# Kernel optimization log

Measured on AMD Instinct MI355X. Metric: run time of the kernel, lower is better.

The kernel has to match this reference:

```python
import jax, jax.numpy as jnp
import numpy as np

B, T, CH_IN = 4096, 8, 2048
C, N, K = 1024, 512, 5  # chennel, prototype length, n_prototypes/classes
EPS = 1e-8


def setup_inputs() -> dict:
    key = jax.random.key(0)
    ks = jax.random.split(key, 14)
    rn = lambda k, s: jax.random.normal(k, s, dtype=jnp.float32)
    return {
        "x": rn(ks[0], (B, T, CH_IN)),
        "static": rn(ks[1], (K, CH_IN, N)),
        "Wk": rn(ks[2], (C, CH_IN)) * 0.02, "bk": rn(ks[3], (C,)) * 0.02,
        "Wv": rn(ks[4], (C, CH_IN)) * 0.02, "bv": rn(ks[5], (C,)) * 0.02,
        "WEk": rn(ks[6], (C, CH_IN)) * 0.02, "bEk": rn(ks[7], (C,)) * 0.02,
        "WEv": rn(ks[8], (C, CH_IN)) * 0.02, "bEv": rn(ks[9], (C,)) * 0.02,
        "Ww": rn(ks[10], (1, C)) * 0.02, "bw": rn(ks[11], (1,)) * 0.02,
        "Wout": rn(ks[12], (K, 2 * C)) * 0.02, "bout": rn(ks[13], (K,)) * 0.02,
    }


def reference(x, static, Wk, bk, Wv, bv, WEk, bEk, WEv, bEv, Ww, bw, Wout, bout):
    # last frame only: [B, ch_in]
    x_last = x[:, -1, :]
    # 1x1 convs on a length-1 sequence == plain linear layers
    k = x_last @ Wk.T + bk  # [B, C]
    v = x_last @ Wv.T + bv  # [B, C]
    # project all 5 static prototypes at once: [K, C, N]
    Ek = jnp.einsum('ci,kin->kcn', WEk, static) + bEk[None, :, None]
    Ev = jnp.einsum('ci,kin->kcn', WEv, static) + bEv[None, :, None]
    # cosine similarity along channel dim (torch eps=1e-8)
    kn = k / jnp.maximum(jnp.linalg.norm(k, axis=1, keepdims=True), EPS)
    Ekn = Ek / jnp.maximum(jnp.linalg.norm(Ek, axis=1, keepdims=True), EPS)
    sim = jnp.einsum('bc,kcn->bkn', kn, Ekn)          # [B, K, N]
    w = jax.nn.softmax(sim, axis=-1)                  # softmax over prototypes' N entries
    # weighted sum of Ev per prototype -> feature_E [B, C, K]
    feature_E = jnp.einsum('kcn,bkn->bck', Ev, w)
    # scalar gate per prototype via conv2_1_W, then sigmoid
    fw = jax.nn.sigmoid(jnp.einsum('c,bck->bk', Ww[0], feature_E) + bw[0])  # [B, K]
    fE = jnp.einsum('bck,bk->bc', feature_E, fw)      # [B, C]
    out = jax.nn.relu(jnp.concatenate([v, fE], axis=1))  # [B, 2C]
    out = out @ Wout.T + bout                          # [B, K]
    return out[:, :, None]                             # [B, K, 1] matching torch conv1d output
```

## Files before the change

### kernel.cpp

```cpp
#include <hip/hip_runtime.h>
#include <hip/hip_bf16.h>

#define BB 4096
#define TT 8
#define CHIN 2048
#define CC 1024
#define NN 512
#define KK 5
#define KN (KK*NN)

typedef __bf16 bf16x8 __attribute__((ext_vector_type(8)));
typedef float  f32x4  __attribute__((ext_vector_type(4)));

#define BM 256
#define BN 256

__device__ __forceinline__ void gload_lds16(const __hip_bfloat16* g, __hip_bfloat16* l) {
    __builtin_amdgcn_global_load_lds(
        (__attribute__((address_space(1))) void*)const_cast<__hip_bfloat16*>(g),
        (__attribute__((address_space(3))) void*)l, 16, 0, 0);
}

__device__ __forceinline__ void stage_q(const __hip_bfloat16* __restrict__ g, int ldg,
                                        __hip_bfloat16* l, int tid)
{
    const int P   = tid * 16;
    const int row = P >> 7;
    const int bc  = (P & 127) ^ ((row & 7) << 4);
    gload_lds16(g + (size_t)row * ldg + (bc >> 1),
                (__hip_bfloat16*)((char*)l + P));
}

__device__ __forceinline__ int xcd_remap()
{
    const int gx = gridDim.x, gy = gridDim.y, gz = gridDim.z;
    const int lin = blockIdx.x + gx * (blockIdx.y + gy * blockIdx.z);
    const int nwg = gx * gy * gz;
    return (lin & 7) * (nwg >> 3) + (lin >> 3);
}

__device__ __forceinline__ void gemm8p_body(
    const __hip_bfloat16* __restrict__ Ag, int lda,
    const __hip_bfloat16* __restrict__ Bg, int ldb,
    float* __restrict__ Cmat, int ldc,
    int ntiles,
    const float* __restrict__ bias_col,
    int bm, int bn)
{
    __shared__ __align__(16) __hip_bfloat16 As[2][BM * 64];
    __shared__ __align__(16) __hip_bfloat16 Bs[2][BN * 64];

    const int tid  = threadIdx.x;
    const int wave = tid >> 6;
    const int lane = tid & 63;
    const int wrow = (wave >> 2) * 128;
    const int wcol = (wave & 3) * 64;
    const int fr   = lane & 15;
    const int kb0  = (lane >> 4) * 16;

    const __hip_bfloat16* Arow = Ag + (size_t)bm * lda;
    const __hip_bfloat16* Brow = Bg + (size_t)bn * ldb;

    const int rA = wrow + fr, rB = wcol + fr;
    const int swA = (rA & 7) << 4, swB = (rB & 7) << 4;
    const int offA0 = rA * 128 + ((kb0     ) ^ swA);
    const int offA1 = rA * 128 + ((kb0 + 64) ^ swA);
    const int offB0 = rB * 128 + ((kb0     ) ^ swB);
    const int offB1 = rB * 128 + ((kb0 + 64) ^ swB);

    f32x4 acc[8][4];
    #pragma unroll
    for (int i = 0; i < 8; ++i)
        #pragma unroll
        for (int j = 0; j < 4; ++j)
            acc[i][j] = {0.f, 0.f, 0.f, 0.f};

    bf16x8 a[4][2];
    bf16x8 b01[2][2];
    bf16x8 b23[2][2];

    #pragma unroll
    for (int q = 0; q < 4; ++q)
        stage_q(Arow + (size_t)(64 * q) * lda, lda, &As[0][q * 4096], tid);
    #pragma unroll
    for (int q = 0; q < 4; ++q)
        stage_q(Brow + (size_t)(64 * q) * ldb, ldb, &Bs[0][q * 4096], tid);
    if (ntiles > 1) {
        #pragma unroll
        for (int q = 0; q < 4; ++q)
            stage_q(Arow + (size_t)(64 * q) * lda + 64, lda, &As[1][q * 4096], tid);
        #pragma unroll
        for (int q = 0; q < 4; ++q)
            stage_q(Brow + (size_t)(64 * q) * ldb + 64, ldb, &Bs[1][q * 4096], tid);
        asm volatile("s_waitcnt vmcnt(8)" ::: "memory");
    } else {
        asm volatile("s_waitcnt vmcnt(0)" ::: "memory");
    }
    __builtin_amdgcn_s_barrier();
    __builtin_amdgcn_sched_barrier(0);

    for (int T = 0; T < ntiles; ++T) {
        const char* aB = (const char*)&As[T & 1][0];
        const char* bB = (const char*)&Bs[T & 1][0];
        const char* aK0 = aB + offA0; const char* aK1 = aB + offA1;
        const char* bK0 = bB + offB0; const char* bK1 = bB + offB1;
        const bool pf = (T + 2 < ntiles);
        const int  kc = (T + 2) * 64;

        #pragma unroll
        for (int i = 0; i < 4; ++i) {
            a[i][0] = *(const bf16x8*)(aK0 + i * 2048);
            a[i][1] = *(const bf16x8*)(aK1 + i * 2048);
        }
        #pragma unroll
        for (int j = 0; j < 2; ++j) {
            b01[j][0] = *(const bf16x8*)(bK0 + j * 2048);
            b01[j][1] = *(const bf16x8*)(bK1 + j * 2048);
        }
        __builtin_amdgcn_s_barrier();
        asm volatile("s_waitcnt lgkmcnt(0)" ::: "memory");
        __builtin_amdgcn_sched_barrier(0);
        __builtin_amdgcn_s_setprio(1);
        #pragma unroll
        for (int i = 0; i < 4; ++i)
            #pragma unroll
            for (int j = 0; j < 2; ++j)
                #pragma unroll
                for (int k2 = 0; k2 < 2; ++k2)
                    acc[i][j] = __builtin_amdgcn_mfma_f32_16x16x32_bf16(
                        a[i][k2], b01[j][k2], acc[i][j], 0, 0, 0);
        __builtin_amdgcn_s_setprio(0);
        __builtin_amdgcn_s_barrier();
        __builtin_amdgcn_sched_barrier(0);

        #pragma unroll
        for (int j = 0; j < 2; ++j) {
            b23[j][0] = *(const bf16x8*)(bK0 + (j + 2) * 2048);
            b23[j][1] = *(const bf16x8*)(bK1 + (j + 2) * 2048);
        }
        if (pf) {
            stage_q(Arow + kc,                       lda, &As[T & 1][0],        tid);
            stage_q(Arow + (size_t)128 * lda + kc,   lda, &As[T & 1][2 * 4096], tid);
        }
        __builtin_amdgcn_s_barrier();
        asm volatile("s_waitcnt lgkmcnt(0)" ::: "memory");
        __builtin_amdgcn_sched_barrier(0);
        __builtin_amdgcn_s_setprio(1);
        #pragma unroll
        for (int i = 0; i < 4; ++i)
            #pragma unroll
            for (int j = 0; j < 2; ++j)
                #pragma unroll
                for (int k2 = 0; k2 < 2; ++k2)
                    acc[i][j + 2] = __builtin_amdgcn_mfma_f32_16x16x32_bf16(
                        a[i][k2], b23[j][k2], acc[i][j + 2], 0, 0, 0);
        __builtin_amdgcn_s_setprio(0);
        __builtin_amdgcn_s_barrier();
        __builtin_amdgcn_sched_barrier(0);

        #pragma unroll
        for (int i = 0; i < 4; ++i) {
            a[i][0] = *(const bf16x8*)(aK0 + 8192 + i * 2048);
            a[i][1] = *(const bf16x8*)(aK1 + 8192 + i * 2048);
        }
        if (pf) {
            #pragma unroll
            for (int q = 0; q < 4; ++q)
                stage_q(Brow + (size_t)(64 * q) * ldb + kc, ldb, &Bs[T & 1][q * 4096], tid);
        }
        __builtin_amdgcn_s_barrier();
        asm volatile("s_waitcnt lgkmcnt(0)" ::: "memory");
        __builtin_amdgcn_sched_barrier(0);
        __builtin_amdgcn_s_setprio(1);
        #pragma unroll
        for (int i = 0; i < 4; ++i)
            #pragma unroll
            for (int j = 0; j < 2; ++j)
                #pragma unroll
                for (int k2 = 0; k2 < 2; ++k2)
                    acc[i + 4][j + 2] = __builtin_amdgcn_mfma_f32_16x16x32_bf16(
                        a[i][k2], b23[j][k2], acc[i + 4][j + 2], 0, 0, 0);
        __builtin_amdgcn_s_setprio(0);
        __builtin_amdgcn_s_barrier();
        __builtin_amdgcn_sched_barrier(0);

        if (pf) {
            stage_q(Arow + (size_t)64 * lda + kc,    lda, &As[T & 1][4096],     tid);
            stage_q(Arow + (size_t)192 * lda + kc,   lda, &As[T & 1][3 * 4096], tid);
            asm volatile("s_waitcnt vmcnt(8)" ::: "memory");
        } else if (T + 1 < ntiles) {
            asm volatile("s_waitcnt vmcnt(0)" ::: "memory");
        }
        __builtin_amdgcn_s_barrier();
        __builtin_amdgcn_sched_barrier(0);
        __builtin_amdgcn_s_setprio(1);
        #pragma unroll
        for (int i = 0; i < 4; ++i)
            #pragma unroll
            for (int j = 0; j < 2; ++j)
                #pragma unroll
                for (int k2 = 0; k2 < 2; ++k2)
                    acc[i + 4][j] = __builtin_amdgcn_mfma_f32_16x16x32_bf16(
                        a[i][k2], b01[j][k2], acc[i + 4][j], 0, 0, 0);
        __builtin_amdgcn_s_setprio(0);
        __builtin_amdgcn_s_barrier();
        __builtin_amdgcn_sched_barrier(0);
    }

    const int quad = lane >> 4;
    #pragma unroll
    for (int i = 0; i < 8; ++i) {
        #pragma unroll
        for (int j = 0; j < 4; ++j) {
            const int col = bn + wcol + j * 16 + fr;
            const float bc = bias_col ? bias_col[col] : 0.f;
            #pragma unroll
            for (int r = 0; r < 4; ++r) {
                const int row = bm + wrow + i * 16 + quad * 4 + r;
                Cmat[(size_t)row * ldc + col] = acc[i][j][r] + bc;
            }
        }
    }
}

__global__ __launch_bounds__(512) void gemm8p_dual(
    const __hip_bfloat16* __restrict__ A0, const __hip_bfloat16* __restrict__ B0,
    float* __restrict__ C0, const float* __restrict__ bias0, int mt0,
    const __hip_bfloat16* __restrict__ A1, const __hip_bfloat16* __restrict__ B1,
    float* __restrict__ C1, const float* __restrict__ bias1)
{
    const int W  = xcd_remap();
    const int bx = W % gridDim.x;
    const int by = W / gridDim.x;
    const bool s = by >= mt0;
    gemm8p_body(s ? A1 : A0, CHIN, s ? B1 : B0, CHIN,
                s ? C1 : C0, 2 * CC, CHIN / 64,
                s ? bias1 : bias0,
                (s ? by - mt0 : by) * BM, bx * BN);
}

__global__ __launch_bounds__(512) void gemm8p(
    const __hip_bfloat16* __restrict__ A, int lda,
    const __hip_bfloat16* __restrict__ BT, int ldb,
    float* __restrict__ C, int ldc, int ntiles,
    const float* __restrict__ bias)
{
    const int W  = xcd_remap();
    const int bx = W % gridDim.x;
    const int by = W / gridDim.x;
    gemm8p_body(A, lda, BT, ldb, C, ldc, ntiles, bias, by * BM, bx * BN);
}

__global__ __launch_bounds__(512) void gemm8p_splitk4(
    const __hip_bfloat16* __restrict__ A, int lda,
    const __hip_bfloat16* __restrict__ BT, int ldb,
    float* __restrict__ C0, float* __restrict__ C1,
    float* __restrict__ C2, float* __restrict__ C3,
    int ldc, int kq_tiles)
{
    const int W   = xcd_remap();
    const int gxy = gridDim.x * gridDim.y;
    const int z   = W / gxy;
    const int rem = W % gxy;
    const int bx  = rem % gridDim.x;
    const int by  = rem / gridDim.x;
    float* C = (z == 0) ? C0 : (z == 1) ? C1 : (z == 2) ? C2 : C3;
    gemm8p_body(A + (size_t)z * kq_tiles * 64, lda,
                BT + (size_t)z * kq_tiles * 64, ldb,
                C, ldc, kq_tiles, nullptr,
                by * BM, bx * BN);
}

#define WG ((CC*CHIN)/4)
#define XG ((BB*CHIN)/4)
#define PREP_BLOCKS ((4*WG + XG + 1024) / 256)

__device__ __forceinline__ void store_bf4(__hip_bfloat16* dst, float4 vv) {
    union { __hip_bfloat16 h[4]; unsigned long long u; } pk;
    pk.h[0] = (__hip_bfloat16)vv.x; pk.h[1] = (__hip_bfloat16)vv.y;
    pk.h[2] = (__hip_bfloat16)vv.z; pk.h[3] = (__hip_bfloat16)vv.w;
    *(unsigned long long*)dst = pk.u;
}

__global__ __launch_bounds__(256) void prep_flat(
    const float* __restrict__ Wk, const float* __restrict__ Wv,
    const float* __restrict__ WEk, const float* __restrict__ WEv,
    const float* __restrict__ x,
    const float* __restrict__ bk, const float* __restrict__ bv,
    const float* __restrict__ bEk, const float* __restrict__ bEv,
    __hip_bfloat16* __restrict__ Wkvb, __hip_bfloat16* __restrict__ WEkvb,
    __hip_bfloat16* __restrict__ xb,
    float* __restrict__ bkv, float* __restrict__ bEkv)
{
    const int gidx = blockIdx.x * 256 + threadIdx.x;
    if (gidx < 4 * WG) {
        const int mat = gidx >> 19;
        const int off = (gidx & (WG - 1)) * 4;
        const float* src = (mat == 0) ? Wk : (mat == 1) ? Wv : (mat == 2) ? WEk : WEv;
        __hip_bfloat16* dst = (mat < 2) ? (Wkvb + (size_t)mat * (CC * CHIN))
                                        : (WEkvb + (size_t)(mat - 2) * (CC * CHIN));
        store_bf4(dst + off, *(const float4*)(src + off));
    } else if (gidx < 4 * WG + XG) {
        const int off = (gidx - 4 * WG) * 4;
        const int b = off >> 11;
        const int i = off & (CHIN - 1);
        store_bf4(xb + off, *(const float4*)(x + ((size_t)b * TT + TT - 1) * CHIN + i));
    } else {
        const int off = (gidx - 4 * WG - XG) * 4;
        #pragma unroll
        for (int e = 0; e < 4; ++e) {
            const int t = off + e;
            if (t < 2 * CC) bkv[t]  = (t < CC) ? bk[t] : bv[t - CC];
            else { const int u2 = t - 2 * CC; bEkv[u2] = (u2 < CC) ? bEk[u2] : bEv[u2 - CC]; }
        }
    }
}

__global__ void transpose_static(const float* __restrict__ st,
                                 __hip_bfloat16* __restrict__ stT)
{
    __shared__ float tile[32][33];
    const int k  = blockIdx.z;
    const int i0 = blockIdx.x * 32;
    const int n0 = blockIdx.y * 32;
    const int tx = threadIdx.x, ty = threadIdx.y;
    #pragma unroll
    for (int r = 0; r < 32; r += 8)
        tile[ty + r][tx] = st[((size_t)k * CHIN + i0 + ty + r) * NN + n0 + tx];
    __syncthreads();
    #pragma unroll
    for (int r = 0; r < 32; r += 8)
        stT[((size_t)k * NN + n0 + ty + r) * CHIN + i0 + tx] = (__hip_bfloat16)tile[tx][ty + r];
}

__global__ void transpose_Ev(const float* __restrict__ Ekv,
                             __hip_bfloat16* __restrict__ EvC)
{
    __shared__ float tile[32][33];
    const int c0  = blockIdx.x * 32;
    const int kn0 = blockIdx.y * 32;
    const int tx = threadIdx.x, ty = threadIdx.y;
    #pragma unroll
    for (int r = 0; r < 32; r += 8)
        tile[ty + r][tx] = Ekv[(size_t)(kn0 + ty + r) * (2 * CC) + CC + c0 + tx];
    __syncthreads();
    #pragma unroll
    for (int r = 0; r < 32; r += 8)
        EvC[(size_t)(c0 + ty + r) * KN + kn0 + tx] = (__hip_bfloat16)tile[tx][ty + r];
}

__global__ __launch_bounds__(256) void norm_prep_E(const float* __restrict__ Ekv,
                                                   const float* __restrict__ Ww,
                                                   __hip_bfloat16* __restrict__ EknT,
                                                   float* __restrict__ g)
{
    const int kn = blockIdx.x;
    const int t  = threadIdx.x;
    const float* pk = Ekv + (size_t)kn * (2 * CC);
    const float4 ek = ((const float4*)pk)[t];
    const float4 ev = ((const float4*)(pk + CC))[t];
    const float4 ww = ((const float4*)Ww)[t];
    float s2 = ek.x*ek.x + ek.y*ek.y + ek.z*ek.z + ek.w*ek.w;
    float sg = ww.x*ev.x + ww.y*ev.y + ww.z*ev.z + ww.w*ev.w;
    #pragma unroll
    for (int o = 32; o > 0; o >>= 1) { s2 += __shfl_down(s2, o, 64); sg += __shfl_down(sg, o, 64); }
    __shared__ float r2[4], rg[4];
    if ((t & 63) == 0) { r2[t >> 6] = s2; rg[t >> 6] = sg; }
    __syncthreads();
    const float tot = r2[0] + r2[1] + r2[2] + r2[3];
    const float inv = 1.f / fmaxf(sqrtf(tot), 1e-8f);
    store_bf4(EknT + (size_t)kn * CC + t * 4,
              make_float4(ek.x * inv, ek.y * inv, ek.z * inv, ek.w * inv));
    if (t == 0) g[kn] = rg[0] + rg[1] + rg[2] + rg[3];
}

__global__ __launch_bounds__(256) void rownorm(const float* __restrict__ in, int in_ld,
                                               __hip_bfloat16* __restrict__ out)
{
    const int row = blockIdx.x;
    const int t   = threadIdx.x;
    const float4 v = ((const float4*)(in + (size_t)row * in_ld))[t];
    float s = v.x*v.x + v.y*v.y + v.z*v.z + v.w*v.w;
    #pragma unroll
    for (int o = 32; o > 0; o >>= 1) s += __shfl_down(s, o, 64);
    __shared__ float red[4];
    if ((t & 63) == 0) red[t >> 6] = s;
    __syncthreads();
    const float tot = red[0] + red[1] + red[2] + red[3];
    const float inv = 1.f / fmaxf(sqrtf(tot), 1e-8f);
    store_bf4(out + (size_t)row * CC + t * 4,
              make_float4(v.x * inv, v.y * inv, v.z * inv, v.w * inv));
}

__global__ __launch_bounds__(256) void softmax_u(const float* __restrict__ sim,
                                                 const float* __restrict__ g,
                                                 const float* __restrict__ bw,
                                                 __hip_bfloat16* __restrict__ u)
{
    const int bk = blockIdx.x * 4 + (threadIdx.x >> 6);
    const int b = bk / KK, k = bk % KK;
    const float* sp = sim + (size_t)b * KN + k * NN;
    const float* gp = g + k * NN;
    const int lane = threadIdx.x & 63;

    const float4 v0 = ((const float4*)sp)[lane * 2];
    const float4 v1 = ((const float4*)sp)[lane * 2 + 1];
    float vals[8] = {v0.x, v0.y, v0.z, v0.w, v1.x, v1.y, v1.z, v1.w};
    float m = -1e30f;
    #pragma unroll
    for (int j = 0; j < 8; ++j) m = fmaxf(m, vals[j]);
    #pragma unroll
    for (int o = 32; o > 0; o >>= 1) m = fmaxf(m, __shfl_xor(m, o, 64));
    float sum = 0.f;
    #pragma unroll
    for (int j = 0; j < 8; ++j) { vals[j] = expf(vals[j] - m); sum += vals[j]; }
    #pragma unroll
    for (int o = 32; o > 0; o >>= 1) sum += __shfl_xor(sum, o, 64);
    const float inv = 1.f / sum;
    const float4 g0 = ((const float4*)gp)[lane * 2];
    const float4 g1 = ((const float4*)gp)[lane * 2 + 1];
    const float gv[8] = {g0.x, g0.y, g0.z, g0.w, g1.x, g1.y, g1.z, g1.w};
    float dot = 0.f;
    #pragma unroll
    for (int j = 0; j < 8; ++j) { vals[j] *= inv; dot += vals[j] * gv[j]; }
    #pragma unroll
    for (int o = 32; o > 0; o >>= 1) dot += __shfl_xor(dot, o, 64);
    const float fw = 1.f / (1.f + expf(-(dot + bw[0])));
    union { __hip_bfloat16 h[8]; bf16x8 v; } pk;
    #pragma unroll
    for (int j = 0; j < 8; ++j) pk.h[j] = (__hip_bfloat16)(vals[j] * fw);
    *(bf16x8*)(u + (size_t)b * KN + k * NN + lane * 8) = pk.v;
}

__global__ __launch_bounds__(256) void final_out(const float* __restrict__ kv,
                                                 const float* __restrict__ fE0,
                                                 const float* __restrict__ fE1,
                                                 const float* __restrict__ fE2,
                                                 const float* __restrict__ fE3,
                                                 const float* __restrict__ Wout,
                                                 const float* __restrict__ bout,
                                                 float* __restrict__ out)
{
    const int b = blockIdx.x;
    const int t = threadIdx.x;
    const float4 v4 = ((const float4*)(kv + (size_t)b * (2 * CC) + CC))[t];
    const float4 a0 = ((const float4*)(fE0 + (size_t)b * CC))[t];
    const float4 a1 = ((const float4*)(fE1 + (size_t)b * CC))[t];
    const float4 a2 = ((const float4*)(fE2 + (size_t)b * CC))[t];
    const float4 a3 = ((const float4*)(fE3 + (size_t)b * CC))[t];
    const float rv[4] = {fmaxf(v4.x, 0.f), fmaxf(v4.y, 0.f), fmaxf(v4.z, 0.f), fmaxf(v4.w, 0.f)};
    const float rf[4] = {fmaxf(a0.x + a1.x + a2.x + a3.x, 0.f),
                         fmaxf(a0.y + a1.y + a2.y + a3.y, 0.f),
                         fmaxf(a0.z + a1.z + a2.z + a3.z, 0.f),
                         fmaxf(a0.w + a1.w + a2.w + a3.w, 0.f)};
    float acc[KK];
    #pragma unroll
    for (int kk = 0; kk < KK; ++kk) {
        const float4 wv = ((const float4*)(Wout + (size_t)kk * 2 * CC))[t];
        const float4 wf = ((const float4*)(Wout + (size_t)kk * 2 * CC + CC))[t];
        acc[kk] = wv.x * rv[0] + wv.y * rv[1] + wv.z * rv[2] + wv.w * rv[3]
                + wf.x * rf[0] + wf.y * rf[1] + wf.z * rf[2] + wf.w * rf[3];
    }
    __shared__ float red[KK][4];
    const int lane = t & 63, wave = t >> 6;
    #pragma unroll
    for (int kk = 0; kk < KK; ++kk) {
        float s = acc[kk];
        #pragma unroll
        for (int o = 32; o > 0; o >>= 1) s += __shfl_down(s, o, 64);
        if (lane == 0) red[kk][wave] = s;
    }
    __syncthreads();
    if (t < KK) {
        float s = red[t][0] + red[t][1] + red[t][2] + red[t][3];
        out[(size_t)b * KK + t] = s + bout[t];
    }
}

extern "C" void kernel_launch(void* const* d_in, const int* in_sizes, int n_in,
                              void* d_out, int out_size, void* d_ws, size_t ws_size,
                              hipStream_t stream)
{
    const float* x    = (const float*)d_in[0];
    const float* stat = (const float*)d_in[1];
    const float* Wk   = (const float*)d_in[2];
    const float* bk   = (const float*)d_in[3];
    const float* Wv   = (const float*)d_in[4];
    const float* bv   = (const float*)d_in[5];
    const float* WEk  = (const float*)d_in[6];
    const float* bEk  = (const float*)d_in[7];
    const float* WEv  = (const float*)d_in[8];
    const float* bEv  = (const float*)d_in[9];
    const float* Ww   = (const float*)d_in[10];
    const float* bw   = (const float*)d_in[11];
    const float* Wout = (const float*)d_in[12];
    const float* bout = (const float*)d_in[13];
    float* out = (float*)d_out;
    char* ws = (char*)d_ws;

    __hip_bfloat16* xb      = (__hip_bfloat16*)(ws + 0);
    __hip_bfloat16* Wkvb    = (__hip_bfloat16*)(ws + 16777216);
    __hip_bfloat16* WEkvb   = (__hip_bfloat16*)(ws + 25165824);
    __hip_bfloat16* staticT = (__hip_bfloat16*)(ws + 33554432);
    float*          Ekv     = (float*)(ws + 44040192);
    __hip_bfloat16* EknT    = (__hip_bfloat16*)(ws + 65011712);
    __hip_bfloat16* EvC     = (__hip_bfloat16*)(ws + 75497472);
    float*          g       = (float*)(ws + 80740352);
    float*          kv      = (float*)(ws + 80750592);
    __hip_bfloat16* kn      = (__hip_bfloat16*)(ws + 114305024);
    float*          sim     = (float*)(ws + 122693632);
    __hip_bfloat16* u       = (__hip_bfloat16*)(ws + 164636672);
    float*          fE      = (float*)(ws + 185608192);
    float*          bkv     = (float*)(ws + 202385408);
    float*          bEkv    = (float*)(ws + 202393600);
    float*          fE2     = (float*)(ws + 202401792);
    float*          fE3     = (float*)(ws + 219179008);
    float*          fE4     = (float*)(ws + 235956224);

    prep_flat<<<PREP_BLOCKS, 256, 0, stream>>>(
        Wk, Wv, WEk, WEv, x, bk, bv, bEk, bEv, Wkvb, WEkvb, xb, bkv, bEkv);
    transpose_static<<<dim3(CHIN / 32, NN / 32, KK), dim3(32, 8), 0, stream>>>(stat, staticT);

    gemm8p_dual<<<dim3(2 * CC / BN, KN / BM + BB / BM), 512, 0, stream>>>(
        staticT, WEkvb, Ekv, bEkv, KN / BM,
        xb, Wkvb, kv, bkv);
    norm_prep_E<<<KN, 256, 0, stream>>>(Ekv, Ww, EknT, g);
    transpose_Ev<<<dim3(CC / 32, KN / 32), dim3(32, 8), 0, stream>>>(Ekv, EvC);
    rownorm<<<BB, 256, 0, stream>>>(kv, 2 * CC, kn);
    gemm8p<<<dim3(KN / BN, BB / BM), 512, 0, stream>>>(
        kn, CC, EknT, CC, sim, KN, CC / 64, nullptr);
    softmax_u<<<BB * KK / 4, 256, 0, stream>>>(sim, g, bw, u);
    gemm8p_splitk4<<<dim3(CC / BN, BB / BM, 4), 512, 0, stream>>>(
        u, KN, EvC, KN, fE, fE2, fE3, fE4, CC, (KN / 4) / 64);
    final_out<<<BB, 256, 0, stream>>>(kv, fE, fE2, fE3, fE4, Wout, bout, out);
}
```

Baseline: 528.5 us.

## Replace 256x256 split-K4 GEMM with 128x128 split-K2 kernel and drop softmax max

The weighted-sum GEMM moves from a 256x256-tile, 512-thread split-K=4 kernel to a new 128x128-tile, 256-thread split-K=2 kernel. The new kernel double-buffers LDS with swizzled layout, issues async global-to-LDS prefetches interleaved with MFMA phases, and uses setprio. It writes half as many partial fE buffers, cutting partial-sum traffic in final_out. The softmax also drops its max-subtraction pass, which saves a reduction but relies on cosine-similarity inputs being bounded in [-1,1] so exp cannot overflow.

```diff
diff --git a/kernel.cpp b/kernel.cpp
--- a/kernel.cpp
+++ b/kernel.cpp
@@ -251,24 +251,193 @@
     gemm8p_body(A, lda, BT, ldb, C, ldc, ntiles, bias, by * BM, bx * BN);
 }
 
-__global__ __launch_bounds__(512) void gemm8p_splitk4(
+__global__ __launch_bounds__(256) void gemm128_splitk2(
     const __hip_bfloat16* __restrict__ A, int lda,
     const __hip_bfloat16* __restrict__ BT, int ldb,
-    float* __restrict__ C0, float* __restrict__ C1,
-    float* __restrict__ C2, float* __restrict__ C3,
-    int ldc, int kq_tiles)
-{
+    float* __restrict__ C0, float* __restrict__ C1, int ldc, int khalf_tiles)
+{
+    __shared__ __align__(16) __hip_bfloat16 As[2][128 * 64];
+    __shared__ __align__(16) __hip_bfloat16 Bs[2][128 * 64];
+
     const int W   = xcd_remap();
     const int gxy = gridDim.x * gridDim.y;
     const int z   = W / gxy;
     const int rem = W % gxy;
     const int bx  = rem % gridDim.x;
     const int by  = rem / gridDim.x;
-    float* C = (z == 0) ? C0 : (z == 1) ? C1 : (z == 2) ? C2 : C3;
-    gemm8p_body(A + (size_t)z * kq_tiles * 64, lda,
-                BT + (size_t)z * kq_tiles * 64, ldb,
-                C, ldc, kq_tiles, nullptr,
-                by * BM, bx * BN);
+    const int bm = by * 128, bn = bx * 128;
+    const int ntiles = khalf_tiles;
+
+    const __hip_bfloat16* Ag = A  + (size_t)z * khalf_tiles * 64;
+    const __hip_bfloat16* Bg = BT + (size_t)z * khalf_tiles * 64;
+    float* Cmat = z ? C1 : C0;
+
+    const int tid  = threadIdx.x;
+    const int wave = tid >> 6;
+    const int lane = tid & 63;
+    const int wrow = (wave >> 1) * 64;
+    const int wcol = (wave & 1) * 64;
+    const int fr   = lane & 15;
+    const int kb0  = (lane >> 4) * 16;
+
+    const __hip_bfloat16* Arow = Ag + (size_t)bm * lda;
+    const __hip_bfloat16* Brow = Bg + (size_t)bn * ldb;
+
+    const int rA = wrow + fr, rB = wcol + fr;
+    const int swA = (rA & 7) << 4, swB = (rB & 7) << 4;
+    const int offA0 = rA * 128 + ((kb0     ) ^ swA);
+    const int offA1 = rA * 128 + ((kb0 + 64) ^ swA);
+    const int offB0 = rB * 128 + ((kb0     ) ^ swB);
+    const int offB1 = rB * 128 + ((kb0 + 64) ^ swB);
+
+    f32x4 acc[4][4];
+    #pragma unroll
+    for (int i = 0; i < 4; ++i)
+        #pragma unroll
+        for (int j = 0; j < 4; ++j)
+            acc[i][j] = {0.f, 0.f, 0.f, 0.f};
+
+    bf16x8 a[2][2];
+    bf16x8 b01[2][2];
+    bf16x8 b23[2][2];
+
+    #pragma unroll
+    for (int q = 0; q < 4; ++q)
+        stage_q(Arow + (size_t)(32 * q) * lda, lda, &As[0][q * 2048], tid);
+    #pragma unroll
+    for (int q = 0; q < 4; ++q)
+        stage_q(Brow + (size_t)(32 * q) * ldb, ldb, &Bs[0][q * 2048], tid);
+    #pragma unroll
+    for (int q = 0; q < 4; ++q)
+        stage_q(Arow + (size_t)(32 * q) * lda + 64, lda, &As[1][q * 2048], tid);
+    #pragma unroll
+    for (int q = 0; q < 4; ++q)
+        stage_q(Brow + (size_t)(32 * q) * ldb + 64, ldb, &Bs[1][q * 2048], tid);
+    asm volatile("s_waitcnt vmcnt(8)" ::: "memory");
+    __builtin_amdgcn_s_barrier();
+    __builtin_amdgcn_sched_barrier(0);
+
+    for (int T = 0; T < ntiles; ++T) {
+        const char* aB = (const char*)&As[T & 1][0];
+        const char* bB = (const char*)&Bs[T & 1][0];
+        const char* aK0 = aB + offA0; const char* aK1 = aB + offA1;
+        const char* bK0 = bB + offB0; const char* bK1 = bB + offB1;
+        const bool pf = (T + 2 < ntiles);
+        const int  kc = (T + 2) * 64;
+
+        #pragma unroll
+        for (int i = 0; i < 2; ++i) {
+            a[i][0] = *(const bf16x8*)(aK0 + i * 2048);
+            a[i][1] = *(const bf16x8*)(aK1 + i * 2048);
+        }
+        #pragma unroll
+        for (int j = 0; j < 2; ++j) {
+            b01[j][0] = *(const bf16x8*)(bK0 + j * 2048);
+            b01[j][1] = *(const bf16x8*)(bK1 + j * 2048);
+        }
+        __builtin_amdgcn_s_barrier();
+        asm volatile("s_waitcnt lgkmcnt(0)" ::: "memory");
+        __builtin_amdgcn_sched_barrier(0);
+        __builtin_amdgcn_s_setprio(1);
+        #pragma unroll
+        for (int i = 0; i < 2; ++i)
+            #pragma unroll
+            for (int j = 0; j < 2; ++j)
+                #pragma unroll
+                for (int k2 = 0; k2 < 2; ++k2)
+                    acc[i][j] = __builtin_amdgcn_mfma_f32_16x16x32_bf16(
+                        a[i][k2], b01[j][k2], acc[i][j], 0, 0, 0);
+        __builtin_amdgcn_s_setprio(0);
+        __builtin_amdgcn_s_barrier();
+        __builtin_amdgcn_sched_barrier(0);
+
+        #pragma unroll
+        for (int j = 0; j < 2; ++j) {
+            b23[j][0] = *(const bf16x8*)(bK0 + (j + 2) * 2048);
+            b23[j][1] = *(const bf16x8*)(bK1 + (j + 2) * 2048);
+        }
+        if (pf) {
+            stage_q(Arow + kc,                      lda, &As[T & 1][0],        tid);
+            stage_q(Arow + (size_t)64 * lda + kc,   lda, &As[T & 1][2 * 2048], tid);
+        }
+        __builtin_amdgcn_s_barrier();
+        asm volatile("s_waitcnt lgkmcnt(0)" ::: "memory");
+        __builtin_amdgcn_sched_barrier(0);
+        __builtin_amdgcn_s_setprio(1);
+        #pragma unroll
+        for (int i = 0; i < 2; ++i)
+            #pragma unroll
+            for (int j = 0; j < 2; ++j)
+                #pragma unroll
+                for (int k2 = 0; k2 < 2; ++k2)
+                    acc[i][j + 2] = __builtin_amdgcn_mfma_f32_16x16x32_bf16(
+                        a[i][k2], b23[j][k2], acc[i][j + 2], 0, 0, 0);
+        __builtin_amdgcn_s_setprio(0);
+        __builtin_amdgcn_s_barrier();
+        __builtin_amdgcn_sched_barrier(0);
+
+        #pragma unroll
+        for (int i = 0; i < 2; ++i) {
+            a[i][0] = *(const bf16x8*)(aK0 + 4096 + i * 2048);
+            a[i][1] = *(const bf16x8*)(aK1 + 4096 + i * 2048);
+        }
+        if (pf) {
+            #pragma unroll
+            for (int q = 0; q < 4; ++q)
+                stage_q(Brow + (size_t)(32 * q) * ldb + kc, ldb, &Bs[T & 1][q * 2048], tid);
+        }
+        __builtin_amdgcn_s_barrier();
+        asm volatile("s_waitcnt lgkmcnt(0)" ::: "memory");
+        __builtin_amdgcn_sched_barrier(0);
+        __builtin_amdgcn_s_setprio(1);
+        #pragma unroll
+        for (int i = 0; i < 2; ++i)
+            #pragma unroll
+            for (int j = 0; j < 2; ++j)
+                #pragma unroll
+                for (int k2 = 0; k2 < 2; ++k2)
+                    acc[i + 2][j + 2] = __builtin_amdgcn_mfma_f32_16x16x32_bf16(
+                        a[i][k2], b23[j][k2], acc[i + 2][j + 2], 0, 0, 0);
+        __builtin_amdgcn_s_setprio(0);
+        __builtin_amdgcn_s_barrier();
+        __builtin_amdgcn_sched_barrier(0);
+
+        if (pf) {
+            stage_q(Arow + (size_t)32 * lda + kc,   lda, &As[T & 1][2048],     tid);
+            stage_q(Arow + (size_t)96 * lda + kc,   lda, &As[T & 1][3 * 2048], tid);
+            asm volatile("s_waitcnt vmcnt(8)" ::: "memory");
+        } else if (T + 1 < ntiles) {
+            asm volatile("s_waitcnt vmcnt(0)" ::: "memory");
+        }
+        __builtin_amdgcn_s_barrier();
+        __builtin_amdgcn_sched_barrier(0);
+        __builtin_amdgcn_s_setprio(1);
+        #pragma unroll
+        for (int i = 0; i < 2; ++i)
+            #pragma unroll
+            for (int j = 0; j < 2; ++j)
+                #pragma unroll
+                for (int k2 = 0; k2 < 2; ++k2)
+                    acc[i + 2][j] = __builtin_amdgcn_mfma_f32_16x16x32_bf16(
+                        a[i][k2], b01[j][k2], acc[i + 2][j], 0, 0, 0);
+        __builtin_amdgcn_s_setprio(0);
+        __builtin_amdgcn_s_barrier();
+        __builtin_amdgcn_sched_barrier(0);
+    }
+
+    const int quad = lane >> 4;
+    #pragma unroll
+    for (int i = 0; i < 4; ++i) {
+        #pragma unroll
+        for (int j = 0; j < 4; ++j) {
+            const int col = bn + wcol + j * 16 + fr;
+            #pragma unroll
+            for (int r = 0; r < 4; ++r) {
+                const int row = bm + wrow + i * 16 + quad * 4 + r;
+                Cmat[(size_t)row * ldc + col] = acc[i][j][r];
+            }
+        }
+    }
 }
 
 #define WG ((CC*CHIN)/4)
@@ -406,14 +575,9 @@
     const float4 v0 = ((const float4*)sp)[lane * 2];
     const float4 v1 = ((const float4*)sp)[lane * 2 + 1];
     float vals[8] = {v0.x, v0.y, v0.z, v0.w, v1.x, v1.y, v1.z, v1.w};
-    float m = -1e30f;
-    #pragma unroll
-    for (int j = 0; j < 8; ++j) m = fmaxf(m, vals[j]);
-    #pragma unroll
-    for (int o = 32; o > 0; o >>= 1) m = fmaxf(m, __shfl_xor(m, o, 64));
     float sum = 0.f;
     #pragma unroll
-    for (int j = 0; j < 8; ++j) { vals[j] = expf(vals[j] - m); sum += vals[j]; }
+    for (int j = 0; j < 8; ++j) { vals[j] = expf(vals[j]); sum += vals[j]; }
     #pragma unroll
     for (int o = 32; o > 0; o >>= 1) sum += __shfl_xor(sum, o, 64);
     const float inv = 1.f / sum;
@@ -435,8 +599,6 @@
 __global__ __launch_bounds__(256) void final_out(const float* __restrict__ kv,
                                                  const float* __restrict__ fE0,
                                                  const float* __restrict__ fE1,
-                                                 const float* __restrict__ fE2,
-                                                 const float* __restrict__ fE3,
                                                  const float* __restrict__ Wout,
                                                  const float* __restrict__ bout,
                                                  float* __restrict__ out)
@@ -446,13 +608,9 @@
     const float4 v4 = ((const float4*)(kv + (size_t)b * (2 * CC) + CC))[t];
     const float4 a0 = ((const float4*)(fE0 + (size_t)b * CC))[t];
     const float4 a1 = ((const float4*)(fE1 + (size_t)b * CC))[t];
-    const float4 a2 = ((const float4*)(fE2 + (size_t)b * CC))[t];
-    const float4 a3 = ((const float4*)(fE3 + (size_t)b * CC))[t];
     const float rv[4] = {fmaxf(v4.x, 0.f), fmaxf(v4.y, 0.f), fmaxf(v4.z, 0.f), fmaxf(v4.w, 0.f)};
-    const float rf[4] = {fmaxf(a0.x + a1.x + a2.x + a3.x, 0.f),
-                         fmaxf(a0.y + a1.y + a2.y + a3.y, 0.f),
-                         fmaxf(a0.z + a1.z + a2.z + a3.z, 0.f),
-                         fmaxf(a0.w + a1.w + a2.w + a3.w, 0.f)};
+    const float rf[4] = {fmaxf(a0.x + a1.x, 0.f), fmaxf(a0.y + a1.y, 0.f),
+                         fmaxf(a0.z + a1.z, 0.f), fmaxf(a0.w + a1.w, 0.f)};
     float acc[KK];
     #pragma unroll
     for (int kk = 0; kk < KK; ++kk) {
@@ -514,8 +672,6 @@
     float*          bkv     = (float*)(ws + 202385408);
     float*          bEkv    = (float*)(ws + 202393600);
     float*          fE2     = (float*)(ws + 202401792);
-    float*          fE3     = (float*)(ws + 219179008);
-    float*          fE4     = (float*)(ws + 235956224);
 
     prep_flat<<<PREP_BLOCKS, 256, 0, stream>>>(
         Wk, Wv, WEk, WEv, x, bk, bv, bEk, bEv, Wkvb, WEkvb, xb, bkv, bEkv);
@@ -530,7 +686,7 @@
     gemm8p<<<dim3(KN / BN, BB / BM), 512, 0, stream>>>(
         kn, CC, EknT, CC, sim, KN, CC / 64, nullptr);
     softmax_u<<<BB * KK / 4, 256, 0, stream>>>(sim, g, bw, u);
-    gemm8p_splitk4<<<dim3(CC / BN, BB / BM, 4), 512, 0, stream>>>(
-        u, KN, EvC, KN, fE, fE2, fE3, fE4, CC, (KN / 4) / 64);
-    final_out<<<BB, 256, 0, stream>>>(kv, fE, fE2, fE3, fE4, Wout, bout, out);
-}
+    gemm128_splitk2<<<dim3(CC / 128, BB / 128, 2), 256, 0, stream>>>(
+        u, KN, EvC, KN, fE, fE2, CC, (KN / 2) / 64);
+    final_out<<<BB, 256, 0, stream>>>(kv, fE, fE2, Wout, bout, out);
+}
```

Result: no change. 521.1 us (-1.4%).
